# Kernel optimization log

Measured on AMD Instinct MI355X. Metric: run time of the kernel, lower is better.

## Reference

```python
import jax, jax.numpy as jnp
import numpy as np

B, S, D, H = 4, 2048, 1024, 16
DK = D // H
NEG = -1.0e9

def setup_inputs() -> dict:
    key = jax.random.key(0)
    ks = jax.random.split(key, 9)
    scale = 1.0 / np.sqrt(D)
    x = jax.random.normal(ks[0], (B, S, D), dtype=jnp.float32)
    # causal mask: positions with mask==0 are filled with -1e9
    mask = jnp.tril(jnp.ones((S, S), dtype=jnp.int32))[None, None]  # [1,1,S,S]
    Wq = jax.random.normal(ks[1], (D, D), dtype=jnp.float32) * scale
    bq = jax.random.normal(ks[2], (D,), dtype=jnp.float32) * 0.01
    Wk = jax.random.normal(ks[3], (D, D), dtype=jnp.float32) * scale
    bk = jax.random.normal(ks[4], (D,), dtype=jnp.float32) * 0.01
    Wv = jax.random.normal(ks[5], (D, D), dtype=jnp.float32) * scale
    bv = jax.random.normal(ks[6], (D,), dtype=jnp.float32) * 0.01
    Wo = jax.random.normal(ks[7], (D, D), dtype=jnp.float32) * scale
    bo = jax.random.normal(ks[8], (D,), dtype=jnp.float32) * 0.01
    return {"x": x, "mask": mask, "Wq": Wq, "bq": bq, "Wk": Wk, "bk": bk,
            "Wv": Wv, "bv": bv, "Wo": Wo, "bo": bo}

def reference(x, mask, Wq, bq, Wk, bk, Wv, bv, Wo, bo):
    Bb, Ss, Dd = x.shape
    q = (x @ Wq.T + bq).reshape(Bb, Ss, H, DK).transpose(0, 2, 1, 3)  # [B,H,S,DK]
    k = (x @ Wk.T + bk).reshape(Bb, Ss, H, DK).transpose(0, 2, 1, 3)
    v = (x @ Wv.T + bv).reshape(Bb, Ss, H, DK).transpose(0, 2, 1, 3)
    scaled = jnp.einsum('bhqd,bhkd->bhqk', q, k) / jnp.sqrt(jnp.float32(DK))
    scaled = jnp.where(mask == 0, jnp.float32(NEG), scaled)
    attn = jax.nn.softmax(scaled, axis=-1)  # dropout prob = 0 -> identity
    vals = jnp.einsum('bhqk,bhkd->bhqd', attn, v)  # [B,H,S,DK]
    vals = vals.transpose(0, 2, 1, 3).reshape(Bb, Ss, H * DK)
    out = vals @ Wo.T + bo
    return out
```

## Files before the change

### kernel.cpp

```cpp
#include <hip/hip_runtime.h>
#include <hip/hip_bf16.h>
#include <cstdint>

#define B_ 4
#define S_ 2048
#define D_ 1024
#define H_ 16
#define DK_ 64

typedef _Float16 h8 __attribute__((ext_vector_type(8)));
typedef _Float16 h4 __attribute__((ext_vector_type(4)));
typedef float f32x4 __attribute__((ext_vector_type(4)));
typedef float f32x16 __attribute__((ext_vector_type(16)));
typedef unsigned int u32x4 __attribute__((ext_vector_type(4)));

__device__ __forceinline__ void gload16(const void* src, void* lds) {
  __builtin_amdgcn_global_load_lds((const __attribute__((address_space(1))) void*)src,
                                   (__attribute__((address_space(3))) void*)lds, 16, 0, 0);
}

__global__ __launch_bounds__(256) void conv_all(
    const float* __restrict__ x,
    const float* __restrict__ Wq, const float* __restrict__ Wk,
    const float* __restrict__ Wv, const float* __restrict__ Wo,
    const float* __restrict__ bq, const float* __restrict__ bk,
    const float* __restrict__ bv,
    _Float16* __restrict__ xb, _Float16* __restrict__ wqkv,
    _Float16* __restrict__ wo, float* __restrict__ bqkv) {
  const int bid = blockIdx.x, tid = threadIdx.x;
  if (bid < 4096) {
    int base = (bid * 256 + tid) * 8;
    h8 o;
#pragma unroll
    for (int j = 0; j < 8; ++j) o[j] = (_Float16)x[base + j];
    *(h8*)(xb + base) = o;
  } else {
    int i = (bid - 4096) * 256 + tid;
    int seg = i >> 17, r = i & 131071;
    const float* src = seg == 0 ? Wq : seg == 1 ? Wk : seg == 2 ? Wv : Wo;
    int base = r * 8;
    h8 o;
#pragma unroll
    for (int j = 0; j < 8; ++j) o[j] = (_Float16)src[base + j];
    if (seg < 3)
      *(h8*)(wqkv + (size_t)seg * 1048576 + base) = o;
    else
      *(h8*)(wo + base) = o;
    if (i < 768) {
      int bsel = i >> 8, k = (i & 255) * 4;
      const float* bs = bsel == 0 ? bq : bsel == 1 ? bk : bv;
      float4 v = *(const float4*)(bs + k);
      *(float4*)(bqkv + bsel * 1024 + k) = v;
    }
  }
}

template <int MODE>
__global__ __launch_bounds__(512, 1) void gemm_pipe(const _Float16* __restrict__ A,
                                                    const _Float16* __restrict__ Bw,
                                                    const float* __restrict__ bias,
                                                    void* __restrict__ Cout,
                                                    _Float16* __restrict__ Vt) {
  __shared__ char lds[2 * 49152];

  const int tid = threadIdx.x;
  const int w = tid >> 6, lane = tid & 63, g = lane >> 4, c = lane & 15;
  const int wm = w >> 1, wn = w & 1;
  const int bn = blockIdx.x;
  const int bm = blockIdx.y;

  f32x4 acc[4][4] = {};

  const int srow = tid >> 3;
  const int scolsw = ((tid & 7) * 16) ^ ((srow & 7) << 4);
  const char* Ab = (const char*)A + (size_t)bm * 256 * 2048;
  const char* Bb = (const char*)Bw + (size_t)bn * 128 * 2048;
  const char* Asrc[4];
  const char* Bsrc[2];
#pragma unroll
  for (int j = 0; j < 4; ++j)
    Asrc[j] = Ab + (size_t)(j * 64 + srow) * 2048 + scolsw;
#pragma unroll
  for (int j = 0; j < 2; ++j)
    Bsrc[j] = Bb + (size_t)(j * 64 + srow) * 2048 + scolsw;

  auto stage = [&](int t) {
    char* slot = lds + (t & 1) * 49152;
    const int k0 = t * 128;
#pragma unroll
    for (int j = 0; j < 4; ++j) gload16(Asrc[j] + k0, slot + j * 8192 + w * 1024);
#pragma unroll
    for (int j = 0; j < 2; ++j) gload16(Bsrc[j] + k0, slot + 32768 + j * 8192 + w * 1024);
  };

  stage(0);

  for (int t = 0; t < 16; ++t) {
    if (t < 15) {
      stage(t + 1);
      asm volatile("s_waitcnt vmcnt(6)" ::: "memory");
    } else {
      asm volatile("s_waitcnt vmcnt(0)" ::: "memory");
    }
    __builtin_amdgcn_s_barrier();
    asm volatile("" ::: "memory");

    const char* slot = lds + (t & 1) * 49152;
#pragma unroll
    for (int kk = 0; kk < 2; ++kk) {
      h8 b[4];
#pragma unroll
      for (int ni = 0; ni < 4; ++ni) {
        int row = wn * 64 + ni * 16 + c;
        int off = row * 128 + kk * 64 + g * 16;
        b[ni] = *(const h8*)(slot + 32768 + (off ^ ((row & 7) << 4)));
      }
      h8 a[4];
#pragma unroll
      for (int mi = 0; mi < 4; ++mi) {
        int row = wm * 64 + mi * 16 + c;
        int off = row * 128 + kk * 64 + g * 16;
        a[mi] = *(const h8*)(slot + (off ^ ((row & 7) << 4)));
      }
      __builtin_amdgcn_s_setprio(1);
#pragma unroll
      for (int mi = 0; mi < 4; ++mi)
#pragma unroll
        for (int ni = 0; ni < 4; ++ni)
          acc[mi][ni] = __builtin_amdgcn_mfma_f32_16x16x32_f16(a[mi], b[ni], acc[mi][ni], 0, 0, 0);
      __builtin_amdgcn_s_setprio(0);
    }

    __builtin_amdgcn_s_barrier();
    asm volatile("" ::: "memory");
  }

  if (MODE == 0 && bn >= 16) {
#pragma unroll
    for (int mi = 0; mi < 4; ++mi)
#pragma unroll
      for (int ni = 0; ni < 4; ++ni) {
        int m0 = bm * 256 + wm * 64 + mi * 16 + g * 4;
        int n = bn * 128 + wn * 64 + ni * 16 + c;
        float bb = bias[n];
        h4 v4;
#pragma unroll
        for (int r = 0; r < 4; ++r) v4[r] = (_Float16)(acc[mi][ni][r] + bb);
        int bI = m0 >> 11, sI = m0 & 2047;
        int dk = n & 63, hh = (n >> 6) & 15;
        *(h4*)(Vt + (((size_t)(bI * 16 + hh) * 64 + dk) * 2048 + sI)) = v4;
      }
  } else {
#pragma unroll
    for (int mi = 0; mi < 4; ++mi)
#pragma unroll
      for (int ni = 0; ni < 4; ++ni)
#pragma unroll
        for (int r = 0; r < 4; ++r) {
          int m = bm * 256 + wm * 64 + mi * 16 + g * 4 + r;
          int n = bn * 128 + wn * 64 + ni * 16 + c;
          float v = acc[mi][ni][r] + bias[n];
          if (MODE == 0) {
            int which = n >> 10, nn = n & 1023;
            int bI = m >> 11, sI = m & 2047, hI = nn >> 6, dkI = nn & 63;
            ((_Float16*)Cout)[(size_t)which * 8388608 +
                              (((size_t)bI * H_ + hI) * S_ + sI) * DK_ + dkI] = (_Float16)v;
          } else {
            ((float*)Cout)[(size_t)m * D_ + n] = v;
          }
        }
  }
}

__global__ __launch_bounds__(512) void attn_fwd(const _Float16* __restrict__ Q,
                                                const _Float16* __restrict__ K,
                                                const _Float16* __restrict__ Vt,
                                                _Float16* __restrict__ vals) {
  __shared__ char lds[3 * 16384];

  const int tid = threadIdx.x;
  const int w = tid >> 6;
  const int lane = tid & 63;
  const int l31 = lane & 31, hi = lane >> 5;
  const int bid = blockIdx.x;
  const int pi = bid >> 6;
  const int bh = bid & 63;
  const int bI = bh >> 4, hI = bh & 15;

  const char* Qb = (const char*)(Q + (size_t)bh * S_ * DK_);
  const char* Kb = (const char*)(K + (size_t)bh * S_ * DK_);
  const char* Vtb = (const char*)(Vt + (size_t)bh * DK_ * S_);

  auto stage = [&](int sloti, int kv0) {
    char* buf = lds + sloti * 16384;
    gload16(Kb + (size_t)kv0 * 128 + (size_t)lane * 128 + w * 16, buf + w * 1024);
    gload16(Vtb + (size_t)lane * 4096 + (size_t)kv0 * 2 + w * 16, buf + 8192 + w * 1024);
  };

  int rdo[4];
#pragma unroll
  for (int ks = 0; ks < 4; ++ks) rdo[ks] = (ks * 2 + hi) * 1024 + l31 * 16;

  const _Float16 qsc = (_Float16)(0.125f * 1.44269504f);

  for (int phase = 0; phase < 2; ++phase) {
    const int sup = (phase == 0) ? pi : 7 - pi;
    const int qw = sup * 8 + w;
    const int nt = 4 * sup + 4;

    h8 qf[4];
#pragma unroll
    for (int ks = 0; ks < 4; ++ks) {
      h8 v = *(const h8*)(Qb + (size_t)(qw * 32 + l31) * 128 + ks * 32 + hi * 16);
#pragma unroll
      for (int j = 0; j < 8; ++j) v[j] *= qsc;
      qf[ks] = v;
    }

    f32x16 o[2] = {};
    float m_ = -1e30f, l_ = 0.f;

    stage(0, 0);
    stage(1, 64);
    asm volatile("s_waitcnt vmcnt(2)" ::: "memory");
    __builtin_amdgcn_s_barrier();
    asm volatile("" ::: "memory");

    for (int t = 0; t < nt; ++t) {
      const char* ldsb = lds + (t % 3) * 16384;
      if (t + 2 < nt) stage((t + 2) % 3, (t + 2) * 64);

      const int rel = qw - 2 * t;
      if (rel >= 0) {
        const bool have1 = (rel >= 1);

        f32x16 s0 = {}, s1 = {};
#pragma unroll
        for (int ks = 0; ks < 4; ++ks) {
          h8 k0 = *(const h8*)(ldsb + rdo[ks]);
          __builtin_amdgcn_s_setprio(1);
          s0 = __builtin_amdgcn_mfma_f32_32x32x16_f16(k0, qf[ks], s0, 0, 0, 0);
          __builtin_amdgcn_s_setprio(0);
          if (have1) {
            h8 k1 = *(const h8*)(ldsb + rdo[ks] + 512);
            __builtin_amdgcn_s_setprio(1);
            s1 = __builtin_amdgcn_mfma_f32_32x32x16_f16(k1, qf[ks], s1, 0, 0, 0);
            __builtin_amdgcn_s_setprio(0);
          }
        }

        if (rel == 0) {
#pragma unroll
          for (int r = 0; r < 16; ++r) {
            int rowidx = (r & 3) + 8 * (r >> 2) + 4 * hi;
            if (rowidx > l31) s0[r] = -1e30f;
          }
        } else if (rel == 1) {
#pragma unroll
          for (int r = 0; r < 16; ++r) {
            int rowidx = (r & 3) + 8 * (r >> 2) + 4 * hi;
            if (rowidx > l31) s1[r] = -1e30f;
          }
        }

        float t8[8];
#pragma unroll
        for (int j = 0; j < 8; ++j) t8[j] = fmaxf(s0[2 * j], s0[2 * j + 1]);
        if (have1)
#pragma unroll
          for (int j = 0; j < 8; ++j) t8[j] = fmaxf(t8[j], fmaxf(s1[2 * j], s1[2 * j + 1]));
        float t4a = fmaxf(t8[0], t8[1]), t4b = fmaxf(t8[2], t8[3]);
        float t4c = fmaxf(t8[4], t8[5]), t4d = fmaxf(t8[6], t8[7]);
        float pmax = fmaxf(fmaxf(t4a, t4b), fmaxf(t4c, t4d));

        if (!__all(pmax <= m_ + 8.f)) {
          float rm = fmaxf(pmax, __shfl_xor(pmax, 32));
          float mn = fmaxf(m_, rm);
          float al = __builtin_amdgcn_exp2f(m_ - mn);
          m_ = mn;
          l_ *= al;
#pragma unroll
          for (int r = 0; r < 16; ++r) {
            float av = __shfl(al, (r & 3) + 8 * (r >> 2) + 4 * hi);
            o[0][r] *= av;
            o[1][r] *= av;
          }
        }

        unsigned int u0[8], u1[8];
        float rsa = 0.f, rsb = 0.f;
#pragma unroll
        for (int j = 0; j < 8; ++j) {
          float e0 = __builtin_amdgcn_exp2f(s0[2 * j] - m_);
          float e1 = __builtin_amdgcn_exp2f(s0[2 * j + 1] - m_);
          rsa += e0 + e1;
          u0[j] = __builtin_bit_cast(unsigned int, __builtin_amdgcn_cvt_pkrtz(e0, e1));
        }
        if (have1) {
#pragma unroll
          for (int j = 0; j < 8; ++j) {
            float e0 = __builtin_amdgcn_exp2f(s1[2 * j] - m_);
            float e1 = __builtin_amdgcn_exp2f(s1[2 * j + 1] - m_);
            rsb += e0 + e1;
            u1[j] = __builtin_bit_cast(unsigned int, __builtin_amdgcn_cvt_pkrtz(e0, e1));
          }
        }
        l_ += rsa + rsb;

        h8 pa0[2], pa1[2];
#pragma unroll
        for (int b = 0; b < 2; ++b) {
          unsigned int ua = u0[4 * b], ub = u0[4 * b + 1];
          unsigned int uc = u0[4 * b + 2], ud = u0[4 * b + 3];
          unsigned int va = hi ? ua : uc, vb = hi ? ub : ud;
          unsigned int xa = __shfl_xor(va, 32), xb = __shfl_xor(vb, 32);
          u32x4 q = {hi ? xa : ua, hi ? xb : ub, hi ? uc : xa, hi ? ud : xb};
          pa0[b] = __builtin_bit_cast(h8, q);
        }
        if (have1) {
#pragma unroll
          for (int b = 0; b < 2; ++b) {
            unsigned int ua = u1[4 * b], ub = u1[4 * b + 1];
            unsigned int uc = u1[4 * b + 2], ud = u1[4 * b + 3];
            unsigned int va = hi ? ua : uc, vb = hi ? ub : ud;
            unsigned int xa = __shfl_xor(va, 32), xb = __shfl_xor(vb, 32);
            u32x4 q = {hi ? xa : ua, hi ? xb : ub, hi ? uc : xa, hi ? ud : xb};
            pa1[b] = __builtin_bit_cast(h8, q);
          }
        }

#pragma unroll
        for (int x = 0; x < 2; ++x) {
#pragma unroll
          for (int kvs = 0; kvs < 4; ++kvs) {
            int ni = kvs >> 1, b = kvs & 1;
            if (!have1 && ni == 1) continue;
            h8 vf = *(const h8*)(ldsb + 8192 + rdo[kvs] + x * 512);
            h8 pa = ni ? pa1[b] : pa0[b];
            __builtin_amdgcn_s_setprio(1);
            o[x] = __builtin_amdgcn_mfma_f32_32x32x16_f16(pa, vf, o[x], 0, 0, 0);
            __builtin_amdgcn_s_setprio(0);
          }
        }
      }

      if (t + 2 < nt)
        asm volatile("s_waitcnt vmcnt(2)" ::: "memory");
      else
        asm volatile("s_waitcnt vmcnt(0)" ::: "memory");
      __builtin_amdgcn_s_barrier();
      asm volatile("" ::: "memory");
    }

    float lt = l_ + __shfl_xor(l_, 32);
    float linv = 1.0f / lt;
#pragma unroll
    for (int r = 0; r < 16; ++r) {
      int qidx = (r & 3) + 8 * (r >> 2) + 4 * hi;
      float inv = __shfl(linv, qidx);
      int qrow = qw * 32 + qidx;
      size_t rowoff = ((size_t)bI * S_ + qrow) * D_ + hI * 64 + l31;
      vals[rowoff] = (_Float16)(o[0][r] * inv);
      vals[rowoff + 32] = (_Float16)(o[1][r] * inv);
    }
  }
}

extern "C" void kernel_launch(void* const* d_in, const int* in_sizes, int n_in,
                              void* d_out, int out_size, void* d_ws, size_t ws_size,
                              hipStream_t stream) {
  const float* x  = (const float*)d_in[0];
  const float* Wq = (const float*)d_in[2];
  const float* bq = (const float*)d_in[3];
  const float* Wk = (const float*)d_in[4];
  const float* bk = (const float*)d_in[5];
  const float* Wv = (const float*)d_in[6];
  const float* bv = (const float*)d_in[7];
  const float* Wo = (const float*)d_in[8];
  const float* bo = (const float*)d_in[9];
  float* out = (float*)d_out;

  char* ws = (char*)d_ws;
  size_t off = 0;
  auto alloc = [&](size_t bytes) {
    char* p = ws + off;
    off += (bytes + 255) & ~(size_t)255;
    return p;
  };
  _Float16* xb   = (_Float16*)alloc((size_t)B_ * S_ * D_ * 2);
  _Float16* wqkv = (_Float16*)alloc((size_t)3 * D_ * D_ * 2);
  _Float16* wob  = (_Float16*)alloc((size_t)D_ * D_ * 2);
  float*    bqkv = (float*)alloc((size_t)3 * D_ * 4);
  _Float16* qkvw = (_Float16*)alloc((size_t)2 * B_ * H_ * S_ * DK_ * 2);
  _Float16* Vtw  = (_Float16*)alloc((size_t)B_ * H_ * S_ * DK_ * 2);
  _Float16* valw = (_Float16*)alloc((size_t)B_ * S_ * D_ * 2);

  conv_all<<<6144, 256, 0, stream>>>(x, Wq, Wk, Wv, Wo, bq, bk, bv, xb, wqkv, wob, bqkv);

  gemm_pipe<0><<<dim3(24, 32), 512, 0, stream>>>(xb, wqkv, bqkv, qkvw, Vtw);

  attn_fwd<<<256, 512, 0, stream>>>(qkvw, qkvw + (size_t)8388608, Vtw, valw);

  gemm_pipe<1><<<dim3(8, 32), 512, 0, stream>>>(valw, wob, bo, out, nullptr);
}
```

Before: 181.3 us.

## Deepen GEMM LDS pipeline to triple buffering and software-pipeline attention QK^T

```diff
diff --git a/kernel.cpp b/kernel.cpp
--- a/kernel.cpp
+++ b/kernel.cpp
@@ -61,7 +61,7 @@
                                                     const float* __restrict__ bias,
                                                     void* __restrict__ Cout,
                                                     _Float16* __restrict__ Vt) {
-  __shared__ char lds[2 * 49152];
+  __shared__ char lds[3 * 49152];
 
   const int tid = threadIdx.x;
   const int w = tid >> 6, lane = tid & 63, g = lane >> 4, c = lane & 15;
@@ -85,7 +85,7 @@
     Bsrc[j] = Bb + (size_t)(j * 64 + srow) * 2048 + scolsw;
 
   auto stage = [&](int t) {
-    char* slot = lds + (t & 1) * 49152;
+    char* slot = lds + (t % 3) * 49152;
     const int k0 = t * 128;
 #pragma unroll
     for (int j = 0; j < 4; ++j) gload16(Asrc[j] + k0, slot + j * 8192 + w * 1024);
@@ -94,10 +94,13 @@
   };
 
   stage(0);
+  stage(1);
 
   for (int t = 0; t < 16; ++t) {
-    if (t < 15) {
-      stage(t + 1);
+    if (t + 2 < 16) {
+      stage(t + 2);
+      asm volatile("s_waitcnt vmcnt(12)" ::: "memory");
+    } else if (t + 1 < 16) {
       asm volatile("s_waitcnt vmcnt(6)" ::: "memory");
     } else {
       asm volatile("s_waitcnt vmcnt(0)" ::: "memory");
@@ -105,7 +108,7 @@
     __builtin_amdgcn_s_barrier();
     asm volatile("" ::: "memory");
 
-    const char* slot = lds + (t & 1) * 49152;
+    const char* slot = lds + (t % 3) * 49152;
 #pragma unroll
     for (int kk = 0; kk < 2; ++kk) {
       h8 b[4];
@@ -176,7 +179,7 @@
                                                 const _Float16* __restrict__ K,
                                                 const _Float16* __restrict__ Vt,
                                                 _Float16* __restrict__ vals) {
-  __shared__ char lds[3 * 16384];
+  __shared__ char lds[4 * 16384];
 
   const int tid = threadIdx.x;
   const int w = tid >> 6;
@@ -202,6 +205,7 @@
   for (int ks = 0; ks < 4; ++ks) rdo[ks] = (ks * 2 + hi) * 1024 + l31 * 16;
 
   const _Float16 qsc = (_Float16)(0.125f * 1.44269504f);
+  const f32x16 vzero = {};
 
   for (int phase = 0; phase < 2; ++phase) {
     const int sup = (phase == 0) ? pi : 7 - pi;
@@ -219,56 +223,64 @@
 
     f32x16 o[2] = {};
     float m_ = -1e30f, l_ = 0.f;
-
-    stage(0, 0);
-    stage(1, 64);
-    asm volatile("s_waitcnt vmcnt(2)" ::: "memory");
-    __builtin_amdgcn_s_barrier();
-    asm volatile("" ::: "memory");
-
-    for (int t = 0; t < nt; ++t) {
-      const char* ldsb = lds + (t % 3) * 16384;
-      if (t + 2 < nt) stage((t + 2) % 3, (t + 2) * 64);
+    f32x16 sA0 = {}, sA1 = {}, sB0 = {}, sB1 = {};
+
+    auto qk = [&](int tn, f32x16& d0, f32x16& d1, bool h1) {
+      const char* ldsb = lds + (tn & 3) * 16384;
+#pragma unroll
+      for (int ks = 0; ks < 4; ++ks) {
+        h8 k0 = *(const h8*)(ldsb + rdo[ks]);
+        __builtin_amdgcn_s_setprio(1);
+        d0 = __builtin_amdgcn_mfma_f32_32x32x16_f16(k0, qf[ks], d0, 0, 0, 0);
+        __builtin_amdgcn_s_setprio(0);
+        if (h1) {
+          h8 k1 = *(const h8*)(ldsb + rdo[ks] + 512);
+          __builtin_amdgcn_s_setprio(1);
+          d1 = __builtin_amdgcn_mfma_f32_32x32x16_f16(k1, qf[ks], d1, 0, 0, 0);
+          __builtin_amdgcn_s_setprio(0);
+        }
+      }
+    };
+
+    auto body = [&](int t, f32x16& c0, f32x16& c1, f32x16& n0, f32x16& n1) {
+      if (t + 2 < nt)
+        asm volatile("s_waitcnt vmcnt(2)" ::: "memory");
+      else
+        asm volatile("s_waitcnt vmcnt(0)" ::: "memory");
+      __builtin_amdgcn_s_barrier();
+      asm volatile("" ::: "memory");
+
+      if (t + 2 < nt) stage((t + 2) & 3, (t + 2) * 64);
+
+      const int reln = qw - 2 * (t + 1);
+      if (t + 1 < nt && reln >= 0) {
+        n0 = vzero; n1 = vzero;
+        qk(t + 1, n0, n1, reln >= 1);
+      }
 
       const int rel = qw - 2 * t;
       if (rel >= 0) {
         const bool have1 = (rel >= 1);
-
-        f32x16 s0 = {}, s1 = {};
-#pragma unroll
-        for (int ks = 0; ks < 4; ++ks) {
-          h8 k0 = *(const h8*)(ldsb + rdo[ks]);
-          __builtin_amdgcn_s_setprio(1);
-          s0 = __builtin_amdgcn_mfma_f32_32x32x16_f16(k0, qf[ks], s0, 0, 0, 0);
-          __builtin_amdgcn_s_setprio(0);
-          if (have1) {
-            h8 k1 = *(const h8*)(ldsb + rdo[ks] + 512);
-            __builtin_amdgcn_s_setprio(1);
-            s1 = __builtin_amdgcn_mfma_f32_32x32x16_f16(k1, qf[ks], s1, 0, 0, 0);
-            __builtin_amdgcn_s_setprio(0);
-          }
-        }
-
         if (rel == 0) {
 #pragma unroll
           for (int r = 0; r < 16; ++r) {
             int rowidx = (r & 3) + 8 * (r >> 2) + 4 * hi;
-            if (rowidx > l31) s0[r] = -1e30f;
+            if (rowidx > l31) c0[r] = -1e30f;
           }
         } else if (rel == 1) {
 #pragma unroll
           for (int r = 0; r < 16; ++r) {
             int rowidx = (r & 3) + 8 * (r >> 2) + 4 * hi;
-            if (rowidx > l31) s1[r] = -1e30f;
+            if (rowidx > l31) c1[r] = -1e30f;
           }
         }
 
         float t8[8];
 #pragma unroll
-        for (int j = 0; j < 8; ++j) t8[j] = fmaxf(s0[2 * j], s0[2 * j + 1]);
+        for (int j = 0; j < 8; ++j) t8[j] = fmaxf(c0[2 * j], c0[2 * j + 1]);
         if (have1)
 #pragma unroll
-          for (int j = 0; j < 8; ++j) t8[j] = fmaxf(t8[j], fmaxf(s1[2 * j], s1[2 * j + 1]));
+          for (int j = 0; j < 8; ++j) t8[j] = fmaxf(t8[j], fmaxf(c1[2 * j], c1[2 * j + 1]));
         float t4a = fmaxf(t8[0], t8[1]), t4b = fmaxf(t8[2], t8[3]);
         float t4c = fmaxf(t8[4], t8[5]), t4d = fmaxf(t8[6], t8[7]);
         float pmax = fmaxf(fmaxf(t4a, t4b), fmaxf(t4c, t4d));
@@ -291,16 +303,16 @@
         float rsa = 0.f, rsb = 0.f;
 #pragma unroll
         for (int j = 0; j < 8; ++j) {
-          float e0 = __builtin_amdgcn_exp2f(s0[2 * j] - m_);
-          float e1 = __builtin_amdgcn_exp2f(s0[2 * j + 1] - m_);
+          float e0 = __builtin_amdgcn_exp2f(c0[2 * j] - m_);
+          float e1 = __builtin_amdgcn_exp2f(c0[2 * j + 1] - m_);
           rsa += e0 + e1;
           u0[j] = __builtin_bit_cast(unsigned int, __builtin_amdgcn_cvt_pkrtz(e0, e1));
         }
         if (have1) {
 #pragma unroll
           for (int j = 0; j < 8; ++j) {
-            float e0 = __builtin_amdgcn_exp2f(s1[2 * j] - m_);
-            float e1 = __builtin_amdgcn_exp2f(s1[2 * j + 1] - m_);
+            float e0 = __builtin_amdgcn_exp2f(c1[2 * j] - m_);
+            float e1 = __builtin_amdgcn_exp2f(c1[2 * j + 1] - m_);
             rsb += e0 + e1;
             u1[j] = __builtin_bit_cast(unsigned int, __builtin_amdgcn_cvt_pkrtz(e0, e1));
           }
@@ -329,13 +341,14 @@
           }
         }
 
+        const char* ldsv = lds + (t & 3) * 16384 + 8192;
 #pragma unroll
         for (int x = 0; x < 2; ++x) {
 #pragma unroll
           for (int kvs = 0; kvs < 4; ++kvs) {
             int ni = kvs >> 1, b = kvs & 1;
             if (!have1 && ni == 1) continue;
-            h8 vf = *(const h8*)(ldsb + 8192 + rdo[kvs] + x * 512);
+            h8 vf = *(const h8*)(ldsv + rdo[kvs] + x * 512);
             h8 pa = ni ? pa1[b] : pa0[b];
             __builtin_amdgcn_s_setprio(1);
             o[x] = __builtin_amdgcn_mfma_f32_32x32x16_f16(pa, vf, o[x], 0, 0, 0);
@@ -343,13 +356,19 @@
           }
         }
       }
-
-      if (t + 2 < nt)
-        asm volatile("s_waitcnt vmcnt(2)" ::: "memory");
-      else
-        asm volatile("s_waitcnt vmcnt(0)" ::: "memory");
-      __builtin_amdgcn_s_barrier();
-      asm volatile("" ::: "memory");
+    };
+
+    stage(0, 0);
+    stage(1, 64);
+    asm volatile("s_waitcnt vmcnt(2)" ::: "memory");
+    __builtin_amdgcn_s_barrier();
+    asm volatile("" ::: "memory");
+    sA0 = vzero; sA1 = vzero;
+    qk(0, sA0, sA1, qw >= 1);
+
+    for (int tt = 0; tt < nt; tt += 2) {
+      body(tt, sA0, sA1, sB0, sB1);
+      body(tt + 1, sB0, sB1, sA0, sA1);
     }
 
     float lt = l_ + __shfl_xor(l_, 32);
```

Result: slower. 452.9 us (+149.8%).
